# Optimization experiments

Measured on AMD Instinct MI355X. Metric: run time of the kernel, lower is better.

## Reference

```python
import jax, jax.numpy as jnp
import numpy as np

LN_EPS = 1e-5

def _dw_conv_dilated(h, w, dil):
    # replicate-pad then VALID dilated depthwise 3x3 conv (groups = channels)
    hp = jnp.pad(h, ((0, 0), (0, 0), (dil, dil), (dil, dil)), mode='edge')
    return jax.lax.conv_general_dilated(
        hp, w, window_strides=(1, 1), padding='VALID', rhs_dilation=(dil, dil),
        dimension_numbers=('NCHW', 'OIHW', 'NCHW'), feature_group_count=h.shape[1])

def setup_inputs() -> dict:
    key = jax.random.key(0)
    ks = jax.random.split(key, 16)
    B, l, d_model = 4, 4096, 512
    d_inner, d_state, dt_rank = 512, 1, 32
    return {
        'x': jax.random.normal(ks[0], (B, l, d_model), jnp.float32),
        'in_proj_w': jax.random.normal(ks[1], (2 * d_inner, d_model), jnp.float32) * 0.02,
        'conv2d_w': jax.random.normal(ks[2], (d_inner, 1, 3, 3), jnp.float32) * 0.1,
        'conv2d_b': jax.random.normal(ks[3], (d_inner,), jnp.float32) * 0.1,
        'x_proj_weight': jax.random.normal(ks[4], (dt_rank + 2 * d_state, d_inner), jnp.float32) * 0.02,
        'dt_projs_weight': jax.random.normal(ks[5], (d_inner, dt_rank), jnp.float32) * 0.1,
        'dt_projs_bias': jax.random.normal(ks[6], (d_inner,), jnp.float32) * 0.1,
        'A_logs': jax.random.normal(ks[7], (d_inner, d_state), jnp.float32),
        'Ds': jax.random.normal(ks[8], (d_inner,), jnp.float32),
        'sf_k3': jax.random.normal(ks[9], (d_inner, 1, 3, 3), jnp.float32) * 0.1,
        'sf_k3_1': jax.random.normal(ks[10], (d_inner, 1, 3, 3), jnp.float32) * 0.1,
        'sf_k3_2': jax.random.normal(ks[11], (d_inner, 1, 3, 3), jnp.float32) * 0.1,
        'sf_alpha': jax.random.normal(ks[12], (3,), jnp.float32),
        'ln_w': jnp.ones((d_inner,), jnp.float32),
        'ln_b': jnp.zeros((d_inner,), jnp.float32),
        'out_proj_w': jax.random.normal(ks[13], (d_model, d_inner), jnp.float32) * 0.02,
    }

def reference(x, in_proj_w, conv2d_w, conv2d_b, x_proj_weight, dt_projs_weight,
              dt_projs_bias, A_logs, Ds, sf_k3, sf_k3_1, sf_k3_2, sf_alpha,
              ln_w, ln_b, out_proj_w):
    B, l, C = x.shape
    sqrt_l = int(np.ceil(np.sqrt(l)))
    new_l = sqrt_l * sqrt_l
    xp = jnp.pad(x, ((0, 0), (0, new_l - l), (0, 0)))
    xg = xp.reshape(B, sqrt_l, sqrt_l, C)                  # b h w c
    xz = xg @ in_proj_w.T                                  # b h w 2d
    d_inner = in_proj_w.shape[0] // 2
    xin, z = xz[..., :d_inner], xz[..., d_inner:]
    xc = jnp.transpose(xin, (0, 3, 1, 2))                  # b d h w
    xc = jax.lax.conv_general_dilated(
        xc, conv2d_w, (1, 1), 'SAME',
        dimension_numbers=('NCHW', 'OIHW', 'NCHW'),
        feature_group_count=d_inner) + conv2d_b[None, :, None, None]
    xc = jax.nn.silu(xc)
    H = W = sqrt_l
    L = H * W
    xs = xc.reshape(B, d_inner, L)                         # b d l
    x_dbl = jnp.einsum('kd,bdl->bkl', x_proj_weight, xs)
    R = dt_projs_weight.shape[1]
    N = A_logs.shape[1]                                    # == 1
    dts = jnp.einsum('dr,brl->bdl', dt_projs_weight, x_dbl[:, :R])
    Bs = x_dbl[:, R:R + N]                                 # b n l
    Cs = x_dbl[:, R + N:R + 2 * N]                         # b n l
    A = -jnp.exp(A_logs)                                   # d n
    delta = jax.nn.softplus(dts + dt_projs_bias[None, :, None])  # b d l
    # selective scan via associative scan: h_t = a_t * h_{t-1} + b_t
    a = jnp.exp(delta[:, :, None, :] * A[None, :, :, None])       # b d n l
    bb = delta[:, :, None, :] * Bs[:, None, :, :] * xs[:, :, None, :]
    def combine(c1, c2):
        a1, b1 = c1
        a2, b2 = c2
        return (a1 * a2, a2 * b1 + b2)
    _, h = jax.lax.associative_scan(combine, (a, bb), axis=-1)
    h = h[:, :, 0, :].reshape(B, d_inner, H, W)            # n == 1
    # StateFusion: 3 dilated replicate-padded depthwise convs
    h = (sf_alpha[0] * _dw_conv_dilated(h, sf_k3, 1)
         + sf_alpha[1] * _dw_conv_dilated(h, sf_k3_1, 2)
         + sf_alpha[2] * _dw_conv_dilated(h, sf_k3_2, 3))
    h = h.reshape(B, d_inner, L)
    y = h * Cs + xs * Ds[None, :, None]                    # Cs (b,1,l) broadcasts
    y = jnp.transpose(y, (0, 2, 1))                        # b l d
    mu = jnp.mean(y, axis=-1, keepdims=True)
    var = jnp.var(y, axis=-1, keepdims=True)
    y = (y - mu) / jnp.sqrt(var + LN_EPS) * ln_w + ln_b
    y = y * jax.nn.silu(z.reshape(B, L, d_inner))
    y = y @ out_proj_w.T
    return y[:, :l, :]
```

## Files before the change

kernel.cpp:

```cpp
#include <hip/hip_runtime.h>
#include <cstddef>


typedef __attribute__((ext_vector_type(8))) short short8;
typedef __attribute__((ext_vector_type(4))) float f32x4;

__device__ __forceinline__ void gload16(const void* g, void* l) {
  __builtin_amdgcn_global_load_lds(
      (const __attribute__((address_space(1))) void*)g,
      (__attribute__((address_space(3))) void*)l, 16, 0, 0);
}

__device__ __forceinline__ void bf16split(float v, unsigned short& h, unsigned short& l) {
  unsigned u = __float_as_uint(v);
  unsigned uh = (u + 0x7fffu + ((u >> 16) & 1u)) & 0xffff0000u;
  h = (unsigned short)(uh >> 16);
  float rem = v - __uint_as_float(uh);
  unsigned ur = __float_as_uint(rem);
  l = (unsigned short)((ur + 0x7fffu + ((ur >> 16) & 1u)) >> 16);
}

__device__ __forceinline__ unsigned short bf16rne(float v) {
  unsigned u = __float_as_uint(v);
  return (unsigned short)((u + 0x7fffu + ((u >> 16) & 1u)) >> 16);
}

__global__ __launch_bounds__(256)
void split_k(const float* __restrict__ in, unsigned short* __restrict__ hi,
             unsigned short* __restrict__ lo, int n4)
{
  int i = blockIdx.x * 256 + threadIdx.x;
  if (i >= n4) return;
  float4 v = ((const float4*)in)[i];
  float vv[4] = {v.x, v.y, v.z, v.w};
  unsigned short h[4], l[4];
#pragma unroll
  for (int j = 0; j < 4; ++j) bf16split(vv[j], h[j], l[j]);
  ((ushort4*)hi)[i] = make_ushort4(h[0], h[1], h[2], h[3]);
  ((ushort4*)lo)[i] = make_ushort4(l[0], l[1], l[2], l[3]);
}

__global__ __launch_bounds__(256)
void cvt_hi_k(const float* __restrict__ in, unsigned short* __restrict__ hi, int n4)
{
  int i = blockIdx.x * 256 + threadIdx.x;
  if (i >= n4) return;
  float4 v = ((const float4*)in)[i];
  ((ushort4*)hi)[i] = make_ushort4(bf16rne(v.x), bf16rne(v.y), bf16rne(v.z), bf16rne(v.w));
}

template<int MODE>
__global__ __launch_bounds__(256)
void gemm_mfma(const unsigned short* __restrict__ Ag_, const unsigned short* __restrict__ Whi,
               const unsigned short* __restrict__ Wlo,
               float* __restrict__ o1, float* __restrict__ o2)
{
  __shared__ char smem[49152];
  unsigned short* sA  = (unsigned short*)smem;
  unsigned short* sBh = (unsigned short*)(smem + 16384);
  unsigned short* sBl = (unsigned short*)(smem + 32768);
  const int tid = threadIdx.x;
  const int wave = tid >> 6, lane = tid & 63;

  const int nwg = gridDim.x;
  const int q = nwg >> 3, r = nwg & 7;
  const int xcd = blockIdx.x & 7, wi = blockIdx.x >> 3;
  const int logical = (xcd < r ? xcd * (q + 1) : r * (q + 1) + (xcd - r) * q) + wi;
  const int NTN = (MODE == 0) ? 8 : 4;
  const int tm = logical / NTN, tn = logical - tm * NTN;
  const int m0 = tm << 7, n0 = tn << 7;

  const int wm = (wave & 1) << 6;
  const int wn = (wave >> 1) << 6;
  const int q16 = (lane >> 4) << 4;
  const int l15 = lane & 15;

  int srow[4], scol[4];
#pragma unroll
  for (int c = 0; c < 4; ++c) {
    int o = (wave << 12) + (c << 10) + (lane << 4);
    int row = o >> 7;
    srow[c] = row;
    scol[c] = (o & 127) ^ ((row & 7) << 4);
  }

  f32x4 acc[4][4];
#pragma unroll
  for (int i = 0; i < 4; ++i)
#pragma unroll
    for (int j = 0; j < 4; ++j) acc[i][j] = (f32x4){0.f, 0.f, 0.f, 0.f};

  for (int kt = 0; kt < 8; ++kt) {
    int kb = kt << 7;
    __syncthreads();
#pragma unroll
    for (int c = 0; c < 4; ++c) {
      size_t ga = (size_t)(m0 + srow[c]) * 1024 + kb + scol[c];
      size_t gb = (size_t)(n0 + srow[c]) * 1024 + kb + scol[c];
      int lo_ = (wave << 12) + (c << 10);
      gload16((const char*)Ag_ + ga, (char*)sA + lo_);
      gload16((const char*)Whi + gb, (char*)sBh + lo_);
      gload16((const char*)Wlo + gb, (char*)sBl + lo_);
    }
    __syncthreads();
#pragma unroll
    for (int ks = 0; ks < 2; ++ks) {
      short8 af[4], bh[4], bl[4];
#pragma unroll
      for (int i = 0; i < 4; ++i) {
        int row = wm + (i << 4) + l15;
        int cb = ((ks << 6) + q16) ^ ((row & 7) << 4);
        af[i] = *(const short8*)((const char*)sA + (row << 7) + cb);
      }
#pragma unroll
      for (int j = 0; j < 4; ++j) {
        int row = wn + (j << 4) + l15;
        int cb = ((ks << 6) + q16) ^ ((row & 7) << 4);
        bh[j] = *(const short8*)((const char*)sBh + (row << 7) + cb);
        bl[j] = *(const short8*)((const char*)sBl + (row << 7) + cb);
      }
#pragma unroll
      for (int i = 0; i < 4; ++i)
#pragma unroll
        for (int j = 0; j < 4; ++j) {
          acc[i][j] = __builtin_amdgcn_mfma_f32_16x16x32_bf16(af[i], bh[j], acc[i][j], 0, 0, 0);
          acc[i][j] = __builtin_amdgcn_mfma_f32_16x16x32_bf16(af[i], bl[j], acc[i][j], 0, 0, 0);
        }
    }
  }

  if (MODE == 0) {
    const int mb_base = m0 + wm + ((lane >> 4) << 2);
#pragma unroll
    for (int j = 0; j < 4; ++j) {
      int n = n0 + wn + (j << 4) + l15;
#pragma unroll
      for (int i = 0; i < 4; ++i) {
        int mb = mb_base + (i << 4);
        if (n < 512) {
          int b = mb >> 12, l = mb & 4095;
          *(f32x4*)&o1[((size_t)(b * 512 + n) << 12) + l] = acc[i][j];
        } else {
#pragma unroll
          for (int rr = 0; rr < 4; ++rr)
            o2[(size_t)(mb + rr) * 512 + (n - 512)] = acc[i][j][rr];
        }
      }
    }
  } else {
    float* sC = (float*)smem;
    const int i_base = (lane >> 4) << 2;
#pragma unroll
    for (int half = 0; half < 2; ++half) {
      __syncthreads();
      if ((wave & 1) == half) {
#pragma unroll
        for (int j = 0; j < 4; ++j) {
          int nl = wn + (j << 4) + l15;
#pragma unroll
          for (int i = 0; i < 4; ++i) {
            int mloc = (i << 4) + i_base;
#pragma unroll
            for (int rr = 0; rr < 4; ++rr)
              sC[(mloc + rr) * 128 + nl] = acc[i][j][rr];
          }
        }
      }
      __syncthreads();
      int cx = (tid & 31) << 2;
      int r0 = tid >> 5;
#pragma unroll
      for (int it = 0; it < 8; ++it) {
        int row = r0 + (it << 3);
        *(float4*)&o1[(size_t)(m0 + (half << 6) + row) * 512 + n0 + cx] =
            *(float4*)&sC[row * 128 + cx];
      }
    }
  }
}

__global__ __launch_bounds__(256)
void conv_silu_k(const float* __restrict__ xin, const float* __restrict__ w,
                 const float* __restrict__ bias, float* __restrict__ xs)
{
  __shared__ float t[64][65];
  int plane = blockIdx.x;
  int d = plane & 511;
  int tid = threadIdx.x;
  const float* src = xin + (size_t)plane * 4096;
#pragma unroll
  for (int i = 0; i < 16; i++) {
    int idx = tid + i * 256;
    t[idx >> 6][idx & 63] = src[idx];
  }
  float wv[9];
#pragma unroll
  for (int j = 0; j < 9; j++) wv[j] = w[d * 9 + j];
  float bv = bias[d];
  __syncthreads();
  float* dst = xs + (size_t)plane * 4096;
#pragma unroll
  for (int i = 0; i < 16; i++) {
    int idx = tid + i * 256;
    int y = idx >> 6, x = idx & 63;
    float s = bv;
#pragma unroll
    for (int u = 0; u < 3; u++)
#pragma unroll
      for (int v = 0; v < 3; v++) {
        int yy = y + u - 1, xx = x + v - 1;
        if (yy >= 0 && yy < 64 && xx >= 0 && xx < 64)
          s = fmaf(wv[u * 3 + v], t[yy][xx], s);
      }
    dst[idx] = s * (1.f / (1.f + __expf(-s)));
  }
}

__global__ __launch_bounds__(256)
void xdbl_part_k(const float* __restrict__ xs, const float* __restrict__ xpw,
                 float* __restrict__ partial)
{
  __shared__ float sw[34 * 64];
  int tid = threadIdx.x;
  int p  = blockIdx.x * 256 + tid;
  int d0 = blockIdx.y * 64;
  int b = p >> 12, l = p & 4095;
  for (int i = tid; i < 34 * 64; i += 256) {
    int k = i >> 6, dd = i & 63;
    sw[i] = xpw[k * 512 + d0 + dd];
  }
  __syncthreads();
  float acc[34];
#pragma unroll
  for (int k = 0; k < 34; k++) acc[k] = 0.f;
  const float* xp = xs + (size_t)(b * 512 + d0) * 4096 + l;
#pragma unroll 4
  for (int dd = 0; dd < 64; dd++) {
    float v = xp[(size_t)dd * 4096];
#pragma unroll
    for (int k = 0; k < 34; k++) acc[k] = fmaf(sw[k * 64 + dd], v, acc[k]);
  }
  float* op = partial + (size_t)blockIdx.y * 34 * 16384 + p;
#pragma unroll
  for (int k = 0; k < 34; k++) op[(size_t)k * 16384] = acc[k];
}

__global__ __launch_bounds__(256)
void xdbl_reduce_k(const float* __restrict__ partial, float* __restrict__ xdbl_r)
{
  int gid = blockIdx.x * 256 + threadIdx.x;
  float s = 0.f;
#pragma unroll
  for (int sp = 0; sp < 8; sp++) s += partial[(size_t)sp * 34 * 16384 + gid];
  xdbl_r[gid] = s;
}

__global__ __launch_bounds__(256)
void delta_k(const float* __restrict__ xdbl_r, const float* __restrict__ dtw,
             const float* __restrict__ dtb, float* __restrict__ del)
{
  __shared__ float sm[32][256];
  int tid = threadIdx.x;
  int l0 = blockIdx.x * 256;
  int d0 = blockIdx.y * 64;
  int b  = blockIdx.z;
  int p0 = b * 4096 + l0;
#pragma unroll
  for (int k = 0; k < 32; k++) sm[k][tid] = xdbl_r[k * 16384 + p0 + tid];
  __syncthreads();
#pragma unroll 2
  for (int dd = 0; dd < 64; dd++) {
    int d = d0 + dd;
    float s = dtb[d];
#pragma unroll
    for (int r = 0; r < 32; r++) s = fmaf(dtw[d * 32 + r], sm[r][tid], s);
    float delta = fmaxf(s, 0.f) + __logf(1.f + __expf(-fabsf(s)));
    del[((size_t)(b * 512 + d) << 12) + l0 + tid] = delta;
  }
}

__global__ __launch_bounds__(256)
void scan_sfconv_k(float* __restrict__ del, const float* __restrict__ Bsr,
                   const float* __restrict__ xs, const float* __restrict__ A_logs,
                   const float* __restrict__ k1, const float* __restrict__ k2,
                   const float* __restrict__ k3, const float* __restrict__ alpha,
                   const float* __restrict__ Cs, const float* __restrict__ Ds)
{
  __shared__ float t[64][65];
  __shared__ float segA[4], segH[4];
  int plane = blockIdx.x;
  int d = plane & 511;
  int b = plane >> 9;
  int tid = threadIdx.x;
  int wave = tid >> 6, lane = tid & 63;
  size_t base = (size_t)plane * 4096;
  float Ad = -__expf(A_logs[d]);

  const int l0 = tid << 4;
  float a_reg[16], b_reg[16];
#pragma unroll
  for (int k = 0; k < 4; ++k) {
    float4 dv4 = *(const float4*)&del[base + l0 + k * 4];
    float4 bs4 = *(const float4*)&Bsr[(b << 12) + l0 + k * 4];
    float4 xs4 = *(const float4*)&xs[base + l0 + k * 4];
    float dv[4] = {dv4.x, dv4.y, dv4.z, dv4.w};
    float bs[4] = {bs4.x, bs4.y, bs4.z, bs4.w};
    float xv[4] = {xs4.x, xs4.y, xs4.z, xs4.w};
#pragma unroll
    for (int j = 0; j < 4; ++j) {
      a_reg[k * 4 + j] = __expf(dv[j] * Ad);
      b_reg[k * 4 + j] = dv[j] * bs[j] * xv[j];
    }
  }

  float A_th = a_reg[0], H_th = b_reg[0];
#pragma unroll
  for (int j = 1; j < 16; ++j) {
    H_th = fmaf(a_reg[j], H_th, b_reg[j]);
    A_th *= a_reg[j];
  }

#pragma unroll
  for (int off = 1; off < 64; off <<= 1) {
    float Ap = __shfl_up(A_th, off);
    float Hp = __shfl_up(H_th, off);
    if (lane >= off) { H_th = fmaf(A_th, Hp, H_th); A_th *= Ap; }
  }
  float eA = __shfl_up(A_th, 1);
  float eH = __shfl_up(H_th, 1);
  if (lane == 0) { eA = 1.f; eH = 0.f; }
  if (lane == 63) { segA[wave] = A_th; segH[wave] = H_th; }
  __syncthreads();

  float cy1 = segH[0];
  float cy2 = fmaf(segA[1], cy1, segH[1]);
  float cy3 = fmaf(segA[2], cy2, segH[2]);
  float myc = (wave == 1) ? cy1 : (wave == 2) ? cy2 : (wave == 3) ? cy3 : 0.f;
  float h = fmaf(eA, myc, eH);

  int row = tid >> 2, col0 = (tid & 3) << 4;
#pragma unroll
  for (int j = 0; j < 16; ++j) {
    h = fmaf(a_reg[j], h, b_reg[j]);
    t[row][col0 + j] = h;
  }
  __syncthreads();

  float wv[3][9];
  float a0 = alpha[0], a1 = alpha[1], a2 = alpha[2];
#pragma unroll
  for (int j = 0; j < 9; j++) {
    wv[0][j] = a0 * k1[d * 9 + j];
    wv[1][j] = a1 * k2[d * 9 + j];
    wv[2][j] = a2 * k3[d * 9 + j];
  }
  float Dv = Ds[d];
  const float* xsp = xs + base;
  const float* Csp = Cs + (b << 12);
  float* yp = del + base;
#pragma unroll
  for (int i = 0; i < 16; i++) {
    int idx = tid + i * 256;
    int y = idx >> 6, x = idx & 63;
    float s = 0.f;
#pragma unroll
    for (int dil = 1; dil <= 3; dil++)
#pragma unroll
      for (int uu = 0; uu < 3; uu++)
#pragma unroll
        for (int vv = 0; vv < 3; vv++) {
          int yy = y + (uu - 1) * dil; yy = yy < 0 ? 0 : (yy > 63 ? 63 : yy);
          int xx = x + (vv - 1) * dil; xx = xx < 0 ? 0 : (xx > 63 ? 63 : xx);
          s = fmaf(wv[dil - 1][uu * 3 + vv], t[yy][xx], s);
        }
    yp[idx] = fmaf(s, Csp[idx], xsp[idx] * Dv);
  }
}

__global__ __launch_bounds__(256)
void transpose_k(const float* __restrict__ src, float* __restrict__ dst)
{
  __shared__ float t[64][65];
  int l0 = blockIdx.x * 64;
  int d0 = blockIdx.y * 64;
  int b  = blockIdx.z;
  int tid = threadIdx.x;
  int c = tid & 63, r4 = tid >> 6;
#pragma unroll
  for (int i = 0; i < 16; i++) {
    int r = r4 + i * 4;
    t[r][c] = src[((size_t)(b * 512 + d0 + r)) * 4096 + l0 + c];
  }
  __syncthreads();
#pragma unroll
  for (int i = 0; i < 16; i++) {
    int r = r4 + i * 4;
    dst[((size_t)(b * 4096 + l0 + r)) * 512 + d0 + c] = t[c][r];
  }
}

__global__ __launch_bounds__(256)
void ln_silu_split_k(const float* __restrict__ y, const float* __restrict__ z,
                     const float* __restrict__ lw, const float* __restrict__ lb,
                     unsigned short* __restrict__ hi)
{
  int wid = threadIdx.x >> 6, lane = threadIdx.x & 63;
  int pix = blockIdx.x * 4 + wid;
  const float* yp = y + (size_t)pix * 512;
  const float* zp = z + (size_t)pix * 512;
  float4 v0 = *(const float4*)&yp[lane * 8];
  float4 v1 = *(const float4*)&yp[lane * 8 + 4];
  float vv[8] = {v0.x,v0.y,v0.z,v0.w,v1.x,v1.y,v1.z,v1.w};
  float sum = 0.f;
#pragma unroll
  for (int j = 0; j < 8; j++) sum += vv[j];
#pragma unroll
  for (int off = 1; off < 64; off <<= 1) sum += __shfl_xor(sum, off);
  float mu = sum * (1.f / 512.f);
  float q = 0.f;
#pragma unroll
  for (int j = 0; j < 8; j++) { float dd = vv[j] - mu; q += dd * dd; }
#pragma unroll
  for (int off = 1; off < 64; off <<= 1) q += __shfl_xor(q, off);
  float rstd = rsqrtf(q * (1.f / 512.f) + 1e-5f);
  float4 z0 = *(const float4*)&zp[lane * 8];
  float4 z1 = *(const float4*)&zp[lane * 8 + 4];
  float zz[8] = {z0.x,z0.y,z0.z,z0.w,z1.x,z1.y,z1.z,z1.w};
  unsigned short oh[8];
#pragma unroll
  for (int j = 0; j < 8; j++) {
    int dch = lane * 8 + j;
    float val = (vv[j] - mu) * rstd * lw[dch] + lb[dch];
    float zv = zz[j];
    float ov = val * (zv * (1.f / (1.f + __expf(-zv))));
    oh[j] = bf16rne(ov);
  }
  size_t o = (size_t)pix * 512 + lane * 8;
  *(ushort4*)&hi[o]     = make_ushort4(oh[0], oh[1], oh[2], oh[3]);
  *(ushort4*)&hi[o + 4] = make_ushort4(oh[4], oh[5], oh[6], oh[7]);
}

extern "C" void kernel_launch(void* const* d_in, const int* in_sizes, int n_in,
                              void* d_out, int out_size, void* d_ws, size_t ws_size,
                              hipStream_t stream)
{
  const float* x    = (const float*)d_in[0];
  const float* win  = (const float*)d_in[1];
  const float* cw   = (const float*)d_in[2];
  const float* cb   = (const float*)d_in[3];
  const float* xpw  = (const float*)d_in[4];
  const float* dtw  = (const float*)d_in[5];
  const float* dtb  = (const float*)d_in[6];
  const float* alog = (const float*)d_in[7];
  const float* Dsv  = (const float*)d_in[8];
  const float* k1   = (const float*)d_in[9];
  const float* k2   = (const float*)d_in[10];
  const float* k3   = (const float*)d_in[11];
  const float* alp  = (const float*)d_in[12];
  const float* lw   = (const float*)d_in[13];
  const float* lb   = (const float*)d_in[14];
  const float* wout = (const float*)d_in[15];
  float* out = (float*)d_out;

  const size_t NP = (size_t)4 * 512 * 4096;
  float* ws = (float*)d_ws;
  float* xs     = ws;
  float* zb     = ws + NP;
  float* w4     = ws + 2 * NP;
  float* xdbl_r = ws + 3 * NP;

  unsigned short* Ahi = (unsigned short*)w4;
  unsigned short* Whi = (unsigned short*)xs;
  unsigned short* Wlo = Whi + (size_t)1024 * 512;
  unsigned short* Yhi = (unsigned short*)w4;
  unsigned short* Ohi = (unsigned short*)xs;
  unsigned short* Olo = Ohi + (size_t)512 * 512;

  cvt_hi_k<<<8192, 256, 0, stream>>>(x, Ahi, 2097152);
  split_k<<<512, 256, 0, stream>>>(win, Whi, Wlo, 131072);
  gemm_mfma<0><<<1024, 256, 0, stream>>>(Ahi, Whi, Wlo, out, zb);
  conv_silu_k<<<2048, 256, 0, stream>>>(out, cw, cb, xs);
  xdbl_part_k<<<dim3(64, 8), 256, 0, stream>>>(xs, xpw, out);
  xdbl_reduce_k<<<2176, 256, 0, stream>>>(out, xdbl_r);
  delta_k<<<dim3(16, 8, 4), 256, 0, stream>>>(xdbl_r, dtw, dtb, w4);
  scan_sfconv_k<<<2048, 256, 0, stream>>>(w4, xdbl_r + 32 * 16384, xs, alog,
                                          k1, k2, k3, alp,
                                          xdbl_r + 33 * 16384, Dsv);
  transpose_k<<<dim3(64, 8, 4), 256, 0, stream>>>(w4, xs);
  ln_silu_split_k<<<4096, 256, 0, stream>>>(xs, zb, lw, lb, Yhi);
  split_k<<<256, 256, 0, stream>>>(wout, Ohi, Olo, 65536);
  gemm_mfma<1><<<512, 256, 0, stream>>>(Yhi, Ohi, Olo, out, nullptr);
}
```

Measured before the change: 208.1 us.

## Store intermediate activations as bf16 to cut memory traffic across stages

The in-projection GEMM now writes its x-branch and z-branch outputs as bf16 instead of fp32. The scan kernel emits its pre-norm output as bf16 in a separate buffer, reading Cs and xs through registers. The transpose and LayerNorm kernels are rewritten to use bf16 with 16-byte vector accesses. This halves the bytes moved through HBM between several memory-bound kernels, at the cost of bf16 rounding on the conv input, the z gate and the LayerNorm input, which may loosen accuracy against the fp32 reference.

Measured after the change: 193.6 us. -7.0%, faster.

```diff
diff --git a/kernel.cpp b/kernel.cpp
--- a/kernel.cpp
+++ b/kernel.cpp
@@ -3,6 +3,7 @@
 
 
 typedef __attribute__((ext_vector_type(8))) short short8;
+typedef __attribute__((ext_vector_type(8))) unsigned short ushort8_t;
 typedef __attribute__((ext_vector_type(4))) float f32x4;
 
 __device__ __forceinline__ void gload16(const void* g, void* l) {
@@ -25,6 +26,10 @@
   return (unsigned short)((u + 0x7fffu + ((u >> 16) & 1u)) >> 16);
 }
 
+__device__ __forceinline__ float b2f(unsigned short u) {
+  return __uint_as_float((unsigned)u << 16);
+}
+
 __global__ __launch_bounds__(256)
 void split_k(const float* __restrict__ in, unsigned short* __restrict__ hi,
              unsigned short* __restrict__ lo, int n4)
@@ -53,7 +58,7 @@
 __global__ __launch_bounds__(256)
 void gemm_mfma(const unsigned short* __restrict__ Ag_, const unsigned short* __restrict__ Whi,
                const unsigned short* __restrict__ Wlo,
-               float* __restrict__ o1, float* __restrict__ o2)
+               void* __restrict__ o1v, void* __restrict__ o2v)
 {
   __shared__ char smem[49152];
   unsigned short* sA  = (unsigned short*)smem;
@@ -130,6 +135,8 @@
   }
 
   if (MODE == 0) {
+    unsigned short* xinb = (unsigned short*)o1v;
+    unsigned short* zb16 = (unsigned short*)o2v;
     const int mb_base = m0 + wm + ((lane >> 4) << 2);
 #pragma unroll
     for (int j = 0; j < 4; ++j) {
@@ -139,15 +146,18 @@
         int mb = mb_base + (i << 4);
         if (n < 512) {
           int b = mb >> 12, l = mb & 4095;
-          *(f32x4*)&o1[((size_t)(b * 512 + n) << 12) + l] = acc[i][j];
+          ushort4 hv = make_ushort4(bf16rne(acc[i][j][0]), bf16rne(acc[i][j][1]),
+                                    bf16rne(acc[i][j][2]), bf16rne(acc[i][j][3]));
+          *(ushort4*)&xinb[((size_t)(b * 512 + n) << 12) + l] = hv;
         } else {
 #pragma unroll
           for (int rr = 0; rr < 4; ++rr)
-            o2[(size_t)(mb + rr) * 512 + (n - 512)] = acc[i][j][rr];
+            zb16[(size_t)(mb + rr) * 512 + (n - 512)] = bf16rne(acc[i][j][rr]);
         }
       }
     }
   } else {
+    float* o1 = (float*)o1v;
     float* sC = (float*)smem;
     const int i_base = (lane >> 4) << 2;
 #pragma unroll
@@ -180,18 +190,21 @@
 }
 
 __global__ __launch_bounds__(256)
-void conv_silu_k(const float* __restrict__ xin, const float* __restrict__ w,
+void conv_silu_k(const unsigned short* __restrict__ xin, const float* __restrict__ w,
                  const float* __restrict__ bias, float* __restrict__ xs)
 {
   __shared__ float t[64][65];
   int plane = blockIdx.x;
   int d = plane & 511;
   int tid = threadIdx.x;
-  const float* src = xin + (size_t)plane * 4096;
-#pragma unroll
-  for (int i = 0; i < 16; i++) {
-    int idx = tid + i * 256;
-    t[idx >> 6][idx & 63] = src[idx];
+  const unsigned short* src = xin + (size_t)plane * 4096;
+  int l0 = tid << 4, row = tid >> 2, c0 = (tid & 3) << 4;
+  ushort8_t v0 = *(const ushort8_t*)&src[l0];
+  ushort8_t v1 = *(const ushort8_t*)&src[l0 + 8];
+#pragma unroll
+  for (int j = 0; j < 8; ++j) {
+    t[row][c0 + j]     = b2f(v0[j]);
+    t[row][c0 + 8 + j] = b2f(v1[j]);
   }
   float wv[9];
 #pragma unroll
@@ -280,11 +293,12 @@
 }
 
 __global__ __launch_bounds__(256)
-void scan_sfconv_k(float* __restrict__ del, const float* __restrict__ Bsr,
+void scan_sfconv_k(const float* __restrict__ del, const float* __restrict__ Bsr,
                    const float* __restrict__ xs, const float* __restrict__ A_logs,
                    const float* __restrict__ k1, const float* __restrict__ k2,
                    const float* __restrict__ k3, const float* __restrict__ alpha,
-                   const float* __restrict__ Cs, const float* __restrict__ Ds)
+                   const float* __restrict__ Cs, const float* __restrict__ Ds,
+                   unsigned short* __restrict__ ypre)
 {
   __shared__ float t[64][65];
   __shared__ float segA[4], segH[4];
@@ -297,7 +311,7 @@
   float Ad = -__expf(A_logs[d]);
 
   const int l0 = tid << 4;
-  float a_reg[16], b_reg[16];
+  float a_reg[16], b_reg[16], x_reg[16];
 #pragma unroll
   for (int k = 0; k < 4; ++k) {
     float4 dv4 = *(const float4*)&del[base + l0 + k * 4];
@@ -310,6 +324,7 @@
     for (int j = 0; j < 4; ++j) {
       a_reg[k * 4 + j] = __expf(dv[j] * Ad);
       b_reg[k * 4 + j] = dv[j] * bs[j] * xv[j];
+      x_reg[k * 4 + j] = xv[j];
     }
   }
 
@@ -338,11 +353,11 @@
   float myc = (wave == 1) ? cy1 : (wave == 2) ? cy2 : (wave == 3) ? cy3 : 0.f;
   float h = fmaf(eA, myc, eH);
 
-  int row = tid >> 2, col0 = (tid & 3) << 4;
+  int row = tid >> 2, c0 = (tid & 3) << 4;
 #pragma unroll
   for (int j = 0; j < 16; ++j) {
     h = fmaf(a_reg[j], h, b_reg[j]);
-    t[row][col0 + j] = h;
+    t[row][c0 + j] = h;
   }
   __syncthreads();
 
@@ -355,13 +370,18 @@
     wv[2][j] = a2 * k3[d * 9 + j];
   }
   float Dv = Ds[d];
-  const float* xsp = xs + base;
-  const float* Csp = Cs + (b << 12);
-  float* yp = del + base;
-#pragma unroll
-  for (int i = 0; i < 16; i++) {
-    int idx = tid + i * 256;
-    int y = idx >> 6, x = idx & 63;
+  float cs_reg[16];
+#pragma unroll
+  for (int k = 0; k < 4; ++k) {
+    float4 c4 = *(const float4*)&Cs[(b << 12) + l0 + k * 4];
+    cs_reg[k * 4 + 0] = c4.x; cs_reg[k * 4 + 1] = c4.y;
+    cs_reg[k * 4 + 2] = c4.z; cs_reg[k * 4 + 3] = c4.w;
+  }
+  unsigned short ov[16];
+  const int y = row;
+#pragma unroll
+  for (int j = 0; j < 16; j++) {
+    int x = c0 + j;
     float s = 0.f;
 #pragma unroll
     for (int dil = 1; dil <= 3; dil++)
@@ -373,44 +393,55 @@
           int xx = x + (vv - 1) * dil; xx = xx < 0 ? 0 : (xx > 63 ? 63 : xx);
           s = fmaf(wv[dil - 1][uu * 3 + vv], t[yy][xx], s);
         }
-    yp[idx] = fmaf(s, Csp[idx], xsp[idx] * Dv);
-  }
-}
-
-__global__ __launch_bounds__(256)
-void transpose_k(const float* __restrict__ src, float* __restrict__ dst)
-{
-  __shared__ float t[64][65];
+    ov[j] = bf16rne(fmaf(s, cs_reg[j], x_reg[j] * Dv));
+  }
+  ushort8_t o0, o1;
+#pragma unroll
+  for (int j = 0; j < 8; ++j) { o0[j] = ov[j]; o1[j] = ov[8 + j]; }
+  *(ushort8_t*)&ypre[base + l0]     = o0;
+  *(ushort8_t*)&ypre[base + l0 + 8] = o1;
+}
+
+__global__ __launch_bounds__(256)
+void transpose_bf16_k(const unsigned short* __restrict__ src,
+                      unsigned short* __restrict__ dst)
+{
+  __shared__ unsigned short t[64][72];
   int l0 = blockIdx.x * 64;
   int d0 = blockIdx.y * 64;
   int b  = blockIdx.z;
   int tid = threadIdx.x;
-  int c = tid & 63, r4 = tid >> 6;
-#pragma unroll
-  for (int i = 0; i < 16; i++) {
-    int r = r4 + i * 4;
-    t[r][c] = src[((size_t)(b * 512 + d0 + r)) * 4096 + l0 + c];
+  int dl = tid & 63, lg0 = tid >> 6;
+#pragma unroll
+  for (int i = 0; i < 2; ++i) {
+    int lg = lg0 + i * 4;
+    ushort8_t v = *(const ushort8_t*)&src[(size_t)(b * 512 + d0 + dl) * 4096 + l0 + lg * 8];
+#pragma unroll
+    for (int j = 0; j < 8; ++j) t[lg * 8 + j][dl] = v[j];
   }
   __syncthreads();
-#pragma unroll
-  for (int i = 0; i < 16; i++) {
-    int r = r4 + i * 4;
-    dst[((size_t)(b * 4096 + l0 + r)) * 512 + d0 + c] = t[c][r];
-  }
-}
-
-__global__ __launch_bounds__(256)
-void ln_silu_split_k(const float* __restrict__ y, const float* __restrict__ z,
+  int pl = tid >> 2, c0 = (tid & 3) << 4;
+  ushort8_t a = *(const ushort8_t*)&t[pl][c0];
+  ushort8_t bb = *(const ushort8_t*)&t[pl][c0 + 8];
+  size_t o = (size_t)(b * 4096 + l0 + pl) * 512 + d0 + c0;
+  *(ushort8_t*)&dst[o] = a;
+  *(ushort8_t*)&dst[o + 8] = bb;
+}
+
+__global__ __launch_bounds__(256)
+void ln_silu_split_k(const unsigned short* __restrict__ y,
+                     const unsigned short* __restrict__ z,
                      const float* __restrict__ lw, const float* __restrict__ lb,
                      unsigned short* __restrict__ hi)
 {
   int wid = threadIdx.x >> 6, lane = threadIdx.x & 63;
   int pix = blockIdx.x * 4 + wid;
-  const float* yp = y + (size_t)pix * 512;
-  const float* zp = z + (size_t)pix * 512;
-  float4 v0 = *(const float4*)&yp[lane * 8];
-  float4 v1 = *(const float4*)&yp[lane * 8 + 4];
-  float vv[8] = {v0.x,v0.y,v0.z,v0.w,v1.x,v1.y,v1.z,v1.w};
+  const unsigned short* yp = y + (size_t)pix * 512;
+  const unsigned short* zp = z + (size_t)pix * 512;
+  ushort8_t yv8 = *(const ushort8_t*)&yp[lane * 8];
+  float vv[8];
+#pragma unroll
+  for (int j = 0; j < 8; j++) vv[j] = b2f(yv8[j]);
   float sum = 0.f;
 #pragma unroll
   for (int j = 0; j < 8; j++) sum += vv[j];
@@ -423,15 +454,13 @@
 #pragma unroll
   for (int off = 1; off < 64; off <<= 1) q += __shfl_xor(q, off);
   float rstd = rsqrtf(q * (1.f / 512.f) + 1e-5f);
-  float4 z0 = *(const float4*)&zp[lane * 8];
-  float4 z1 = *(const float4*)&zp[lane * 8 + 4];
-  float zz[8] = {z0.x,z0.y,z0.z,z0.w,z1.x,z1.y,z1.z,z1.w};
+  ushort8_t zv8 = *(const ushort8_t*)&zp[lane * 8];
   unsigned short oh[8];
 #pragma unroll
   for (int j = 0; j < 8; j++) {
     int dch = lane * 8 + j;
     float val = (vv[j] - mu) * rstd * lw[dch] + lb[dch];
-    float zv = zz[j];
+    float zv = b2f(zv8[j]);
     float ov = val * (zv * (1.f / (1.f + __expf(-zv))));
     oh[j] = bf16rne(ov);
   }
@@ -465,29 +494,33 @@
   const size_t NP = (size_t)4 * 512 * 4096;
   float* ws = (float*)d_ws;
   float* xs     = ws;
-  float* zb     = ws + NP;
+  float* zbuf   = ws + NP;
   float* w4     = ws + 2 * NP;
   float* xdbl_r = ws + 3 * NP;
 
-  unsigned short* Ahi = (unsigned short*)w4;
-  unsigned short* Whi = (unsigned short*)xs;
-  unsigned short* Wlo = Whi + (size_t)1024 * 512;
-  unsigned short* Yhi = (unsigned short*)w4;
-  unsigned short* Ohi = (unsigned short*)xs;
-  unsigned short* Olo = Ohi + (size_t)512 * 512;
+  unsigned short* Ahi  = (unsigned short*)w4;
+  unsigned short* Whi  = (unsigned short*)xs;
+  unsigned short* Wlo  = Whi + (size_t)1024 * 512;
+  unsigned short* xinb = (unsigned short*)d_out;
+  unsigned short* zb16 = (unsigned short*)zbuf;
+  unsigned short* yp16 = zb16 + (size_t)16384 * 512;
+  unsigned short* yt16 = (unsigned short*)xs;
+  unsigned short* Yhi  = (unsigned short*)w4;
+  unsigned short* Ohi  = (unsigned short*)xs;
+  unsigned short* Olo  = Ohi + (size_t)512 * 512;
 
   cvt_hi_k<<<8192, 256, 0, stream>>>(x, Ahi, 2097152);
   split_k<<<512, 256, 0, stream>>>(win, Whi, Wlo, 131072);
-  gemm_mfma<0><<<1024, 256, 0, stream>>>(Ahi, Whi, Wlo, out, zb);
-  conv_silu_k<<<2048, 256, 0, stream>>>(out, cw, cb, xs);
+  gemm_mfma<0><<<1024, 256, 0, stream>>>(Ahi, Whi, Wlo, xinb, zb16);
+  conv_silu_k<<<2048, 256, 0, stream>>>(xinb, cw, cb, xs);
   xdbl_part_k<<<dim3(64, 8), 256, 0, stream>>>(xs, xpw, out);
   xdbl_reduce_k<<<2176, 256, 0, stream>>>(out, xdbl_r);
   delta_k<<<dim3(16, 8, 4), 256, 0, stream>>>(xdbl_r, dtw, dtb, w4);
   scan_sfconv_k<<<2048, 256, 0, stream>>>(w4, xdbl_r + 32 * 16384, xs, alog,
                                           k1, k2, k3, alp,
-                                          xdbl_r + 33 * 16384, Dsv);
-  transpose_k<<<dim3(64, 8, 4), 256, 0, stream>>>(w4, xs);
-  ln_silu_split_k<<<4096, 256, 0, stream>>>(xs, zb, lw, lb, Yhi);
+                                          xdbl_r + 33 * 16384, Dsv, yp16);
+  transpose_bf16_k<<<dim3(64, 8, 4), 256, 0, stream>>>(yp16, yt16);
+  ln_silu_split_k<<<4096, 256, 0, stream>>>(yt16, zb16, lw, lb, Yhi);
   split_k<<<256, 256, 0, stream>>>(wout, Ohi, Olo, 65536);
   gemm_mfma<1><<<512, 256, 0, stream>>>(Yhi, Ohi, Olo, out, nullptr);
 }
```
